# Kernel optimization log

Measured on AMD Instinct MI355X. Metric: run time of the kernel, lower is better.

Reference implementation:

```python
import jax, jax.numpy as jnp
import numpy as np

V, B, NP, NJ = 5, 32, 20, 17
NB = 16
ND = 128
POSE_MIN_DEPTH, POSE_MAX_DEPTH = 2000.0, 8000.0
POSE_SIGMA = 100.0
KS = 11
HIDDEN_ROUGH, HIDDEN = 1024, 1024
BONES = np.array([[0,1],[0,2],[1,3],[2,4],[5,6],[5,7],[7,9],[6,8],[8,10],[5,11],[6,12],[11,12],[11,13],[13,15],[12,14],[14,16]], dtype=np.int32)


def setup_inputs() -> dict:
    key = jax.random.key(0)
    ks = jax.random.split(key, 12)
    wh = jnp.array([1920.0, 1080.0], jnp.float32)
    kpts = jax.random.uniform(ks[0], (V, B, NP, NJ, 2), jnp.float32) * wh
    pose_vis = jnp.ones((V, B, NP), jnp.float32)
    joint_vis = (jax.random.uniform(ks[1], (V, B, NP, NJ)) > 0.15).astype(jnp.float32)
    gt_pose_depths = jax.random.uniform(ks[2], (B, NP), jnp.float32, 2000.0, 8000.0)
    gt_joint_depths = jax.random.uniform(ks[3], (B, NP, NJ), jnp.float32, -100.0, 100.0)
    angles = np.linspace(-0.3, 0.3, V)
    Rs = np.stack([np.array([[np.cos(a), 0.0, np.sin(a)], [0.0, 1.0, 0.0], [-np.sin(a), 0.0, np.cos(a)]], dtype=np.float32) for a in angles])
    cam_R = jnp.broadcast_to(jnp.asarray(Rs)[:, None], (V, B, 3, 3))
    tvec = np.zeros((V, 3), np.float32); tvec[:, 0] = np.linspace(-500.0, 500.0, V)
    cam_T = jnp.broadcast_to(jnp.asarray(tvec)[:, None], (V, B, 3))
    cam_f = jnp.full((V, B, 2), 1400.0, jnp.float32)
    cam_c = jnp.broadcast_to(jnp.array([960.0, 540.0], jnp.float32), (V, B, 2))
    image_wh = jnp.broadcast_to(jnp.array([1920.0, 1080.0], jnp.float32), (V, B, 2))
    num_persons = jax.random.randint(ks[4], (V, B), 10, NP + 1, jnp.int32)
    Wr1 = jax.random.normal(ks[5], (HIDDEN_ROUGH, NJ * 2)) * 0.02
    br1 = jnp.zeros((HIDDEN_ROUGH,), jnp.float32)
    Wr2 = jax.random.normal(ks[6], (NJ, HIDDEN_ROUGH)) * 0.02
    br2 = jnp.zeros((NJ,), jnp.float32)
    Wc1 = jax.random.normal(ks[7], (HIDDEN, NJ + NB, 3)) * 0.02
    bc1 = jnp.zeros((HIDDEN,), jnp.float32)
    Wc2 = jax.random.normal(ks[8], (1, HIDDEN, 3)) * 0.02
    bc2 = jnp.zeros((1,), jnp.float32)
    bones = jnp.asarray(BONES)
    return dict(kpts=kpts, pose_vis=pose_vis, joint_vis=joint_vis, gt_pose_depths=gt_pose_depths, gt_joint_depths=gt_joint_depths, cam_R=cam_R, cam_T=cam_T, cam_f=cam_f, cam_c=cam_c, image_wh=image_wh, num_persons=num_persons, Wr1=Wr1, br1=br1, Wr2=Wr2, br2=br2, Wc1=Wc1, bc1=bc1, Wc2=Wc2, bc2=bc2, bones=bones)


def _bone_len(p, bones):
    # p: [B, Np, Nj, D, 2] -> [B, Np, Nb, D]
    a = p[:, :, bones[:, 0]]
    b = p[:, :, bones[:, 1]]
    return jnp.sqrt(jnp.sum((a - b) ** 2, -1) + 1e-12)


def _conv1d(x, w, b):
    # x [N,C,L], w [O,I,3]
    y = jax.lax.conv_general_dilated(x, w, (1,), 'SAME', dimension_numbers=('NCH', 'OIH', 'NCH'))
    return y + b[None, :, None]


def _forward(kpts, joint_vis, cam_R, cam_T, cam_f, cam_c, image_wh, num_persons, Wr1, br1, Wr2, br2, Wc1, bc1, Wc2, bc2, bones):
    V_, B_, NP_, NJ_, _ = kpts.shape
    labels = jnp.arange(ND, dtype=jnp.float32) / (ND - 1) * (POSE_MAX_DEPTH - POSE_MIN_DEPTH) + POSE_MIN_DEPTH
    kt = kpts[0]  # target-view 2D poses [B,Np,Nj,2]
    # faithful to original indexing quirk: normalize all batches by batch-0 image size
    kn = kt / image_wh[0, 0][None, None, None, :]
    x = kn.reshape(B_ * NP_, NJ_ * 2)
    h = jax.nn.relu(x @ Wr1.T + br1)
    rough = (h @ Wr2.T + br2).reshape(B_, NP_, NJ_) * 1000.0
    rough = jax.lax.stop_gradient(rough)  # .detach() in original
    depths = labels[None, None, None, :] + rough[..., None]  # [B,Np,Nj,D]
    # back-project target 2D poses at every depth hypothesis
    R0, T0, f0, c0 = cam_R[0], cam_T[0], cam_f[0], cam_c[0]
    uvn = (kt - c0[:, None, None, :]) / f0[:, None, None, :]
    xy = uvn[..., None, :] * depths[..., None]
    cam_pts = jnp.concatenate([xy, depths[..., None]], -1)
    p3d = jnp.einsum('bji,bpkdj->bpkdi', R0, cam_pts) + T0[:, None, None, None, :]  # world [B,Np,Nj,D,3]

    scores = scores2 = boundings = boundings2 = None
    for rv in range(1, V_):
        Rr, Tr, fr, cr = cam_R[rv], cam_T[rv], cam_f[rv], cam_c[rv]
        xc = jnp.einsum('bij,bpkdj->bpkdi', Rr, p3d - Tr[:, None, None, None, :])
        p2t = xc[..., :2] / (xc[..., 2:3] + 1e-8) * fr[:, None, None, None, :] + cr[:, None, None, None, :]
        pr = kpts[rv]         # [B,Npr,Nj,2]
        vr = joint_vis[rv]    # [B,Npr,Nj]
        # pairwise dist over (target-person, ref-person) per joint/depth
        d = jnp.sum((p2t[:, :, None] - pr[:, None, :, :, None, :]) ** 2, -1)  # [B,Npt,Npr,Nj,D]
        w = vr[:, None, :, :, None]
        pdist = jnp.sum(d * w, 3) / (jnp.sum(w, 3) + 1e-8)  # [B,Npt,Npr,D]
        valid = jnp.arange(NP_)[None, None, :, None] < num_persons[rv][:, None, None, None]
        pdist = jnp.where(valid, pdist, 1e5)
        mm = jnp.argmin(pdist, 2)  # [B,Npt,D] nearest ref pose
        bidx = jnp.arange(B_)[:, None, None]
        matched = jnp.transpose(pr[bidx, mm], (0, 1, 3, 2, 4))  # [B,Npt,Nj,D,2]
        mvis = jnp.transpose(vr[bidx, mm], (0, 1, 3, 2))        # [B,Npt,Nj,D]
        mdist = jnp.sum((p2t - matched) ** 2, -1)
        score = jnp.exp(-jnp.sqrt(mdist + 1e-12) / POSE_SIGMA)  # panoptic branch
        score_bl = jnp.exp(-jnp.abs(_bone_len(matched, bones) - _bone_len(p2t, bones)) / 5.0)
        wimg = image_wh[rv][:, None, None, None, 0]
        himg = image_wh[rv][:, None, None, None, 1]
        inb = ((p2t[..., 0] >= 0) & (p2t[..., 1] >= 0) & (p2t[..., 0] <= wimg - 1) & (p2t[..., 1] <= himg - 1)).astype(score.dtype)
        bounding = inb * mvis
        bounding2 = jnp.broadcast_to(mvis[:, :, :1, :], score_bl.shape)
        if scores is None:
            scores, scores2 = score * bounding, score_bl * bounding2
            boundings, boundings2 = bounding, bounding2
        else:
            scores = scores + score * bounding
            scores2 = scores2 + score_bl * bounding2
            boundings = boundings + bounding
            boundings2 = boundings2 + bounding2
    psv = (scores / (boundings + 1e-8)).reshape(B_ * NP_, NJ_, ND)
    psv2 = (scores2 / (boundings2 + 1e-8)).reshape(B_ * NP_, NB, ND)
    xin = jnp.concatenate([psv, psv2], 1)  # [BN, Nj+Nb, D]
    hc = jax.nn.relu(_conv1d(xin, Wc1, bc1))
    logits = _conv1d(hc, Wc2, bc2)[:, 0, :]  # [BN, D]
    vol = jax.nn.softmax(logits, -1)
    # soft-argmax restricted to a window around the argmax
    pos = jnp.arange(ND, dtype=vol.dtype)
    idx = jnp.argmax(vol, -1)
    mask = (jnp.abs(pos[None, :] - idx[:, None].astype(vol.dtype)) <= KS // 2).astype(vol.dtype)
    mv = vol * mask
    mv = mv / (jnp.sum(mv, -1, keepdims=True) + 1e-8)
    pred_idx = jnp.sum(mv * pos, -1).reshape(B_, NP_)
    return pred_idx / (ND - 1) * (POSE_MAX_DEPTH - POSE_MIN_DEPTH) + POSE_MIN_DEPTH


def reference(kpts, pose_vis, joint_vis, gt_pose_depths, gt_joint_depths, cam_R, cam_T, cam_f, cam_c, image_wh, num_persons, Wr1, br1, Wr2, br2, Wc1, bc1, Wc2, bc2, bones):
    return _forward(kpts, joint_vis, cam_R, cam_T, cam_f, cam_c, image_wh, num_persons, Wr1, br1, Wr2, br2, Wc1, bc1, Wc2, bc2, bones)
```

## Files before the change

kernel.cpp:

```cpp
#include <hip/hip_runtime.h>
#include <math.h>

#define VV  5
#define BB  32
#define NPP 20
#define NJJ 17
#define NBB 16
#define NDD 128
#define HID 1024
#define KPITCH 128
#define PRP 36
#define VRP 20
#define NCH 34
#define RGH_P 20
#define BASE_P 52
#define A2_ELEMS (64 * 4 * 64 * 8)
#define EPI2_ELEMS (64 * 64 * 16)

typedef __attribute__((ext_vector_type(8))) short short8;
typedef __attribute__((ext_vector_type(4))) float floatx4;

static constexpr int BONE_A[NBB] = {0,0,1,2,5,5,7,6,8,5,6,11,11,13,12,14};
static constexpr int BONE_B[NBB] = {1,2,3,4,6,7,9,8,10,11,12,12,13,15,14,16};

__device__ __forceinline__ float warp_red_sum(float v) {
#pragma unroll
  for (int off = 32; off >= 1; off >>= 1) v += __shfl_xor(v, off, 64);
  return v;
}

__global__ __launch_bounds__(256) void prep_kernel(
    const float* __restrict__ Wc1, const float* __restrict__ Wc2,
    const float* __restrict__ bc1,
    unsigned short* __restrict__ A_hi, unsigned short* __restrict__ A_lo,
    float* __restrict__ epi) {
  int gidx = blockIdx.x * 256 + threadIdx.x;
  if (gidx < A2_ELEMS) {
    int e = gidx & 7;
    int l = (gidx >> 3) & 63;
    int rest = gidx >> 9;
    int ks = rest & 3;
    int ot = rest >> 2;
    int o = ot * 16 + (l & 15);
    int kk = ks * 32 + (l >> 4) * 8 + e;
    float x = (kk < 99) ? Wc1[o * 99 + kk] : 0.0f;
    unsigned int u = __float_as_uint(x);
    unsigned short hi = (unsigned short)(u >> 16);
    float xh = __uint_as_float((u >> 16) << 16);
    unsigned short lo = (unsigned short)(__float_as_uint(x - xh) >> 16);
    A_hi[gidx] = hi;
    A_lo[gidx] = lo;
  } else {
    int idx2 = gidx - A2_ELEMS;
    if (idx2 < EPI2_ELEMS) {
      int c = idx2 & 15;
      int l = (idx2 >> 4) & 63;
      int ot = idx2 >> 10;
      int base = ot * 16 + (l >> 4) * 4;
      epi[idx2] = (c < 12) ? Wc2[(base + c / 3) * 3 + (c % 3)] : bc1[base + (c - 12)];
    }
  }
}

__global__ __launch_bounds__(256) void pose_pre_kernel(
    const float* __restrict__ kpts, const float* __restrict__ cam_R,
    const float* __restrict__ cam_f, const float* __restrict__ cam_c,
    const float* __restrict__ image_wh,
    const float* __restrict__ Wr1, const float* __restrict__ br1,
    const float* __restrict__ Wr2, const float* __restrict__ br2,
    float* __restrict__ ws_rough, float* __restrict__ ws_base) {
  const int n = blockIdx.x;
  const int b = n / NPP;
  const int p = n % NPP;
  const int tid = threadIdx.x;
  const int wv = tid >> 6, ln = tid & 63;

  __shared__ float sh_x[NJJ * 2];
  __shared__ float sh_h[HID];

  if (tid < NJJ * 2) {
    int j = tid >> 1, c = tid & 1;
    float k = kpts[((size_t)(b * NPP + p)) * NJJ * 2 + j * 2 + c];
    sh_x[tid] = k / image_wh[c];
  }
  __syncthreads();

#pragma unroll
  for (int k = 0; k < 4; ++k) {
    int m = tid + k * 256;
    float acc = br1[m];
#pragma unroll
    for (int c = 0; c < NJJ * 2; ++c) acc = fmaf(Wr1[m * (NJJ * 2) + c], sh_x[c], acc);
    sh_h[m] = fmaxf(acc, 0.0f);
  }
  __syncthreads();

  for (int j = wv; j < NJJ; j += 4) {
    float part = 0.0f;
    for (int m = ln; m < HID; m += 64) part = fmaf(Wr2[j * HID + m], sh_h[m], part);
    part = warp_red_sum(part);
    if (ln == 0) ws_rough[(size_t)n * RGH_P + j] = (part + br2[j]) * 1000.0f;
  }

  if (tid < NJJ) {
    int j = tid;
    const float* R0 = cam_R + (size_t)b * 9;
    float c0x = cam_c[b * 2 + 0], c0y = cam_c[b * 2 + 1];
    float f0x = cam_f[b * 2 + 0], f0y = cam_f[b * 2 + 1];
    float kx = kpts[((size_t)(b * NPP + p)) * NJJ * 2 + j * 2 + 0];
    float ky = kpts[((size_t)(b * NPP + p)) * NJJ * 2 + j * 2 + 1];
    float ux = (kx - c0x) / f0x;
    float uy = (ky - c0y) / f0y;
#pragma unroll
    for (int i = 0; i < 3; ++i)
      ws_base[(size_t)n * BASE_P + j * 3 + i] =
          R0[0 * 3 + i] * ux + R0[1 * 3 + i] * uy + R0[2 * 3 + i];
  }
}

__global__ __launch_bounds__(256, 4) void pose_match_kernel(
    const float* __restrict__ kpts, const float* __restrict__ joint_vis,
    const float* __restrict__ cam_R, const float* __restrict__ cam_T,
    const float* __restrict__ cam_f, const float* __restrict__ cam_c,
    const float* __restrict__ image_wh, const int* __restrict__ num_persons,
    const float* __restrict__ ws_rough, const float* __restrict__ ws_base,
    float* __restrict__ ws_partial) {
  const int bid = blockIdx.x;
  const int n = bid >> 1;
  const int bh = bid & 1;
  const int b = n / NPP;
  const int tid = threadIdx.x;
  const int rvv = tid >> 6;
  const int d = bh * 64 + (tid & 63);

  __shared__ float sh_rough[NJJ];
  __shared__ float sh_base[NJJ][3];
  __shared__ __align__(16) float sh_pr[4][NPP][PRP];
  __shared__ __align__(16) float sh_vr[4][NPP][VRP];

  if (tid < NJJ) sh_rough[tid] = ws_rough[(size_t)n * RGH_P + tid];
  if (tid >= 64 && tid < 64 + NJJ * 3)
    ((float*)sh_base)[tid - 64] = ws_base[(size_t)n * BASE_P + (tid - 64)];

#pragma unroll
  for (int rr = 0; rr < 4; ++rr) {
    const float* prg = kpts + ((size_t)(rr + 1) * BB + b) * NPP * NJJ * 2;
    for (int idx = tid; idx < NPP * NJJ * 2; idx += 256)
      sh_pr[rr][idx / 34][idx % 34] = prg[idx];
    const float* vrg = joint_vis + ((size_t)(rr + 1) * BB + b) * NPP * NJJ;
    for (int idx = tid; idx < NPP * NJJ; idx += 256)
      sh_vr[rr][idx / 17][idx % 17] = vrg[idx];
  }
  if (tid < 4 * BB) {
    int rr = tid >> 5, q = tid & 31;
    if (q < NPP) {
      sh_pr[rr][q][34] = 0.0f; sh_pr[rr][q][35] = 0.0f;
      sh_vr[rr][q][17] = 0.0f; sh_vr[rr][q][18] = 0.0f; sh_vr[rr][q][19] = 0.0f;
    }
  }
  __syncthreads();

  {
    const int rv = rvv + 1;
    const int vb = rv * BB + b;
    const float* Rr = cam_R + (size_t)vb * 9;
    const float R00 = Rr[0], R01 = Rr[1], R02 = Rr[2];
    const float R10 = Rr[3], R11 = Rr[4], R12 = Rr[5];
    const float R20 = Rr[6], R21 = Rr[7], R22 = Rr[8];
    const float Trx = cam_T[vb * 3 + 0], Try = cam_T[vb * 3 + 1], Trz = cam_T[vb * 3 + 2];
    const float frx = cam_f[vb * 2 + 0], fry = cam_f[vb * 2 + 1];
    const float crx = cam_c[vb * 2 + 0], cry = cam_c[vb * 2 + 1];
    const float wmax = image_wh[vb * 2 + 0] - 1.0f;
    const float hmax = image_wh[vb * 2 + 1] - 1.0f;
    const int nprv = num_persons[vb];
    const float T0x = cam_T[b * 3 + 0], T0y = cam_T[b * 3 + 1], T0z = cam_T[b * 3 + 2];
    const float lab = ((float)d / 127.0f) * 6000.0f + 2000.0f;

    float px[NJJ], py[NJJ];
#pragma unroll
    for (int j = 0; j < NJJ; ++j) {
      float dep = lab + sh_rough[j];
      float p0 = fmaf(dep, sh_base[j][0], T0x);
      float p1 = fmaf(dep, sh_base[j][1], T0y);
      float p2 = fmaf(dep, sh_base[j][2], T0z);
      float q0 = p0 - Trx, q1 = p1 - Try, q2 = p2 - Trz;
      float xc0 = R00 * q0 + R01 * q1 + R02 * q2;
      float xc1 = R10 * q0 + R11 * q1 + R12 * q2;
      float xc2 = R20 * q0 + R21 * q1 + R22 * q2 + 1e-8f;
      px[j] = xc0 / xc2 * frx + crx;
      py[j] = xc1 / xc2 * fry + cry;
    }

    float best = 3.4e38f;
    int mm = 0;
#pragma unroll 1
    for (int q = 0; q < NPP; ++q) {
      const float4* pr4 = (const float4*)(&sh_pr[rvv][q][0]);
      const float4* vr4 = (const float4*)(&sh_vr[rvv][q][0]);
      float num = 0.0f, den = 0.0f;
#pragma unroll
      for (int g4 = 0; g4 < 4; ++g4) {
        float4 w  = vr4[g4];
        float4 pa = pr4[2 * g4 + 0];
        float4 pb = pr4[2 * g4 + 1];
        { float dx = px[4*g4+0] - pa.x, dy = py[4*g4+0] - pa.y; num = fmaf(w.x, dx*dx + dy*dy, num); den += w.x; }
        { float dx = px[4*g4+1] - pa.z, dy = py[4*g4+1] - pa.w; num = fmaf(w.y, dx*dx + dy*dy, num); den += w.y; }
        { float dx = px[4*g4+2] - pb.x, dy = py[4*g4+2] - pb.y; num = fmaf(w.z, dx*dx + dy*dy, num); den += w.z; }
        { float dx = px[4*g4+3] - pb.z, dy = py[4*g4+3] - pb.w; num = fmaf(w.w, dx*dx + dy*dy, num); den += w.w; }
      }
      {
        float w16 = sh_vr[rvv][q][16];
        float4 pc = pr4[8];
        float dx = px[16] - pc.x, dy = py[16] - pc.y;
        num = fmaf(w16, dx*dx + dy*dy, num); den += w16;
      }
      float pd = num / (den + 1e-8f);
      if (q >= nprv) pd = 100000.0f;
      if (pd < best) { best = pd; mm = q; }
    }

    float* pbase = ws_partial + (((size_t)n * NCH) * 4 + rvv) * 128 + d;
    unsigned int maskB = 0u;
#pragma unroll
    for (int j = 0; j < NJJ; ++j) {
      float mx = sh_pr[rvv][mm][j * 2 + 0];
      float my = sh_pr[rvv][mm][j * 2 + 1];
      float mv = sh_vr[rvv][mm][j];
      float dx = px[j] - mx, dy = py[j] - my;
      float sc = expf(-sqrtf(dx * dx + dy * dy + 1e-12f) / 100.0f);
      float inb = (px[j] >= 0.0f && py[j] >= 0.0f && px[j] <= wmax && py[j] <= hmax) ? 1.0f : 0.0f;
      float bd = inb * mv;
      pbase[j * 512] = sc * bd;
      maskB |= ((unsigned int)(bd != 0.0f)) << j;
    }
    float v0 = sh_vr[rvv][mm][0];
    maskB |= ((unsigned int)(v0 != 0.0f)) << 17;
#pragma unroll
    for (int nb = 0; nb < NBB; ++nb) {
      const int a = BONE_A[nb], c = BONE_B[nb];
      float ax = sh_pr[rvv][mm][a * 2 + 0], ay = sh_pr[rvv][mm][a * 2 + 1];
      float cx = sh_pr[rvv][mm][c * 2 + 0], cy = sh_pr[rvv][mm][c * 2 + 1];
      float dmx = ax - cx, dmy = ay - cy;
      float blm = sqrtf(dmx * dmx + dmy * dmy + 1e-12f);
      float dpx = px[a] - px[c], dpy = py[a] - py[c];
      float blp = sqrtf(dpx * dpx + dpy * dpy + 1e-12f);
      float scb = expf(-fabsf(blm - blp) / 5.0f);
      pbase[(NJJ + nb) * 512] = scb * v0;
    }
    *(unsigned int*)(pbase + 33 * 512) = maskB;
  }
}

__global__ __launch_bounds__(128) void reduce_kernel(
    const float* __restrict__ ws_partial, float* __restrict__ ws_xin) {
  const int n = blockIdx.x;
  const int t = threadIdx.x;
  const float* pb = ws_partial + ((size_t)n * NCH) * 4 * 128;
  float* xo = ws_xin + (size_t)n * (NJJ + NBB) * NDD;

  unsigned int m0 = __float_as_uint(pb[(33 * 4 + 0) * 128 + t]);
  unsigned int m1 = __float_as_uint(pb[(33 * 4 + 1) * 128 + t]);
  unsigned int m2 = __float_as_uint(pb[(33 * 4 + 2) * 128 + t]);
  unsigned int m3 = __float_as_uint(pb[(33 * 4 + 3) * 128 + t]);

#pragma unroll
  for (int i = 0; i < NJJ; ++i) {
    const float* a = pb + (i * 4) * 128 + t;
    float s = ((a[0] + a[128]) + a[256]) + a[384];
    int bj = ((m0 >> i) & 1) + ((m1 >> i) & 1) + ((m2 >> i) & 1) + ((m3 >> i) & 1);
    xo[i * NDD + t] = s / ((float)bj + 1e-8f);
  }
  int b2 = ((m0 >> 17) & 1) + ((m1 >> 17) & 1) + ((m2 >> 17) & 1) + ((m3 >> 17) & 1);
  float den2 = (float)b2 + 1e-8f;
#pragma unroll
  for (int nb = 0; nb < NBB; ++nb) {
    const float* a = pb + ((NJJ + nb) * 4) * 128 + t;
    float s = ((a[0] + a[128]) + a[256]) + a[384];
    xo[(NJJ + nb) * NDD + t] = s / den2;
  }
}

__global__ __launch_bounds__(512, 2) void conv_mfma_kernel(
    const float* __restrict__ ws_xin,
    const unsigned short* __restrict__ A_hi, const unsigned short* __restrict__ A_lo,
    const float* __restrict__ epi,
    const float* __restrict__ bc2, float* __restrict__ out) {
  const int n = blockIdx.x;
  const int tid = threadIdx.x;
  const int w = tid >> 6;
  const int l = tid & 63;
  const int lcol = l & 15;
  const int lg = l >> 4;

  __shared__ __align__(16) unsigned short bT_hi[128 * KPITCH];
  __shared__ __align__(16) unsigned short bT_lo[128 * KPITCH];
  __shared__ float plg[3][8][NDD];
  __shared__ float sh_l[NDD];
  __shared__ float sh_e[NDD];
  __shared__ float sh_sc[2];

  for (int i = tid; i < 3 * 8 * NDD; i += 512) ((float*)plg)[i] = 0.0f;

  const float* xn = ws_xin + (size_t)n * (NJJ + NBB) * NDD;
  for (int idx = tid; idx < 64 * 128; idx += 512) {
    const int kp = (idx & 63) << 1;
    const int t  = idx >> 6;
    unsigned int hp = 0, lp = 0;
#pragma unroll
    for (int u = 0; u < 2; ++u) {
      const int kk = kp + u;
      float x = 0.0f;
      if (kk < 99) {
        int i3 = kk / 3;
        int k3 = kk - i3 * 3;
        int tt = t + k3 - 1;
        if (tt >= 0 && tt < 128) x = xn[i3 * NDD + tt];
      }
      unsigned int uu = __float_as_uint(x);
      unsigned int hi = uu >> 16;
      float xh = __uint_as_float(hi << 16);
      unsigned int lo = __float_as_uint(x - xh) >> 16;
      hp |= hi << (16 * u);
      lp |= lo << (16 * u);
    }
    const int e = t * KPITCH + (kp ^ ((t & 15) << 3));
    *(unsigned int*)(bT_hi + e) = hp;
    *(unsigned int*)(bT_lo + e) = lp;
  }
  __syncthreads();

  const int sw = lcol << 3;

#pragma unroll 1
  for (int oi = 0; oi < 8; ++oi) {
    const int otg = w * 8 + oi;

    short8 Ah[4], Al[4];
    {
      const short8* ahT = ((const short8*)A_hi) + (size_t)otg * 4 * 64 + l;
      const short8* alT = ((const short8*)A_lo) + (size_t)otg * 4 * 64 + l;
#pragma unroll
      for (int ks = 0; ks < 4; ++ks) {
        Ah[ks] = ahT[ks * 64];
        Al[ks] = alT[ks * 64];
      }
    }
    float w2f[12];
    float bcf[4];
    {
      const float4* ep = ((const float4*)epi) + ((size_t)otg * 64 + l) * 4;
      float4 e0 = ep[0], e1 = ep[1], e2 = ep[2], e3 = ep[3];
      w2f[0] = e0.x; w2f[1] = e0.y; w2f[2] = e0.z; w2f[3] = e0.w;
      w2f[4] = e1.x; w2f[5] = e1.y; w2f[6] = e1.z; w2f[7] = e1.w;
      w2f[8] = e2.x; w2f[9] = e2.y; w2f[10] = e2.z; w2f[11] = e2.w;
      bcf[0] = e3.x; bcf[1] = e3.y; bcf[2] = e3.z; bcf[3] = e3.w;
    }

#pragma unroll 1
    for (int tp = 0; tp < 4; ++tp) {
      const int t0 = tp * 32 + lcol;
      const int t1 = t0 + 16;
      const unsigned short* b0h = bT_hi + t0 * KPITCH;
      const unsigned short* b1h = bT_hi + t1 * KPITCH;
      const unsigned short* b0l = bT_lo + t0 * KPITCH;
      const unsigned short* b1l = bT_lo + t1 * KPITCH;

      floatx4 X0 = {0.f, 0.f, 0.f, 0.f}, Y0 = {0.f, 0.f, 0.f, 0.f};
      floatx4 X1 = {0.f, 0.f, 0.f, 0.f}, Y1 = {0.f, 0.f, 0.f, 0.f};

#pragma unroll
      for (int ks = 0; ks < 4; ++ks) {
        const int e = (ks * 32 + lg * 8) ^ sw;
        short8 bh0 = *(const short8*)(b0h + e);
        short8 bh1 = *(const short8*)(b1h + e);
        X0 = __builtin_amdgcn_mfma_f32_16x16x32_bf16(Ah[ks], bh0, X0, 0, 0, 0);
        Y0 = __builtin_amdgcn_mfma_f32_16x16x32_bf16(Al[ks], bh0, Y0, 0, 0, 0);
        X1 = __builtin_amdgcn_mfma_f32_16x16x32_bf16(Ah[ks], bh1, X1, 0, 0, 0);
        Y1 = __builtin_amdgcn_mfma_f32_16x16x32_bf16(Al[ks], bh1, Y1, 0, 0, 0);
      }
#pragma unroll
      for (int ks = 0; ks < 4; ++ks) {
        const int e = (ks * 32 + lg * 8) ^ sw;
        short8 bl0 = *(const short8*)(b0l + e);
        short8 bl1 = *(const short8*)(b1l + e);
        if (ks & 1) {
          Y0 = __builtin_amdgcn_mfma_f32_16x16x32_bf16(Ah[ks], bl0, Y0, 0, 0, 0);
          Y1 = __builtin_amdgcn_mfma_f32_16x16x32_bf16(Ah[ks], bl1, Y1, 0, 0, 0);
        } else {
          X0 = __builtin_amdgcn_mfma_f32_16x16x32_bf16(Ah[ks], bl0, X0, 0, 0, 0);
          X1 = __builtin_amdgcn_mfma_f32_16x16x32_bf16(Ah[ks], bl1, X1, 0, 0, 0);
        }
      }

      {
        float sP = 0.0f, sC = 0.0f, sM = 0.0f;
#pragma unroll
        for (int r = 0; r < 4; ++r) {
          float h = fmaxf((X0[r] + Y0[r]) + bcf[r], 0.0f);
          sP = fmaf(h, w2f[r * 3 + 0], sP);
          sC = fmaf(h, w2f[r * 3 + 1], sC);
          sM = fmaf(h, w2f[r * 3 + 2], sM);
        }
        sP += __shfl_xor(sP, 16, 64); sP += __shfl_xor(sP, 32, 64);
        sC += __shfl_xor(sC, 16, 64); sC += __shfl_xor(sC, 32, 64);
        sM += __shfl_xor(sM, 16, 64); sM += __shfl_xor(sM, 32, 64);
        if (lg == 0) {
          plg[0][w][t0] += sP;
          plg[1][w][t0] += sC;
          plg[2][w][t0] += sM;
        }
      }
      {
        float sP = 0.0f, sC = 0.0f, sM = 0.0f;
#pragma unroll
        for (int r = 0; r < 4; ++r) {
          float h = fmaxf((X1[r] + Y1[r]) + bcf[r], 0.0f);
          sP = fmaf(h, w2f[r * 3 + 0], sP);
          sC = fmaf(h, w2f[r * 3 + 1], sC);
          sM = fmaf(h, w2f[r * 3 + 2], sM);
        }
        sP += __shfl_xor(sP, 16, 64); sP += __shfl_xor(sP, 32, 64);
        sC += __shfl_xor(sC, 16, 64); sC += __shfl_xor(sC, 32, 64);
        sM += __shfl_xor(sM, 16, 64); sM += __shfl_xor(sM, 32, 64);
        if (lg == 0) {
          plg[0][w][t1] += sP;
          plg[1][w][t1] += sC;
          plg[2][w][t1] += sM;
        }
      }
    }
  }
  __syncthreads();

  if (tid < NDD) {
    int t = tid;
    float lg2 = bc2[0];
#pragma unroll
    for (int ww = 0; ww < 8; ++ww) lg2 += plg[1][ww][t];
    if (t > 0) {
#pragma unroll
      for (int ww = 0; ww < 8; ++ww) lg2 += plg[0][ww][t - 1];
    }
    if (t < NDD - 1) {
#pragma unroll
      for (int ww = 0; ww < 8; ++ww) lg2 += plg[2][ww][t + 1];
    }
    sh_l[t] = lg2;
  }
  __syncthreads();
  if (tid < 64) {
    float v1 = sh_l[tid], v2 = sh_l[tid + 64];
    float mv; int mi;
    if (v2 > v1) { mv = v2; mi = tid + 64; } else { mv = v1; mi = tid; }
#pragma unroll
    for (int off = 32; off >= 1; off >>= 1) {
      float ov = __shfl_xor(mv, off, 64);
      int   oi2 = __shfl_xor(mi, off, 64);
      if (ov > mv || (ov == mv && oi2 < mi)) { mv = ov; mi = oi2; }
    }
    if (tid == 0) { sh_sc[0] = mv; ((int*)sh_sc)[1] = mi; }
  }
  __syncthreads();
  const float gmax = sh_sc[0];
  const int gidx = ((const int*)sh_sc)[1];
  if (tid < NDD) sh_e[tid] = expf(sh_l[tid] - gmax);
  __syncthreads();
  if (tid < 64) {
    float S = warp_red_sum(sh_e[tid] + sh_e[tid + 64]);
    float a1 = 0.0f, a2 = 0.0f;
#pragma unroll
    for (int k = 0; k < 2; ++k) {
      int t = tid + k * 64;
      float vol = sh_e[t] / S;
      float msk = (fabsf((float)t - (float)gidx) <= 5.0f) ? 1.0f : 0.0f;
      float mvv = vol * msk;
      a1 += mvv;
      a2 += mvv * (float)t;
    }
    a1 = warp_red_sum(a1);
    a2 = warp_red_sum(a2);
    if (tid == 0) {
      float pred = a2 / (a1 + 1e-8f);
      out[n] = pred / 127.0f * 6000.0f + 2000.0f;
    }
  }
}

extern "C" void kernel_launch(void* const* d_in, const int* in_sizes, int n_in,
                              void* d_out, int out_size, void* d_ws, size_t ws_size,
                              hipStream_t stream) {
  (void)in_sizes; (void)n_in; (void)out_size; (void)ws_size;
  const float* kpts        = (const float*)d_in[0];
  const float* joint_vis   = (const float*)d_in[2];
  const float* cam_R       = (const float*)d_in[5];
  const float* cam_T       = (const float*)d_in[6];
  const float* cam_f       = (const float*)d_in[7];
  const float* cam_c       = (const float*)d_in[8];
  const float* image_wh    = (const float*)d_in[9];
  const int*   num_persons = (const int*)d_in[10];
  const float* Wr1 = (const float*)d_in[11];
  const float* br1 = (const float*)d_in[12];
  const float* Wr2 = (const float*)d_in[13];
  const float* br2 = (const float*)d_in[14];
  const float* Wc1 = (const float*)d_in[15];
  const float* bc1 = (const float*)d_in[16];
  const float* Wc2 = (const float*)d_in[17];
  const float* bc2 = (const float*)d_in[18];
  float* out = (float*)d_out;

  unsigned short* A_hi = (unsigned short*)d_ws;
  unsigned short* A_lo = A_hi + A2_ELEMS;
  float* epi        = (float*)(A_lo + A2_ELEMS);
  float* ws_xin     = epi + EPI2_ELEMS;
  float* ws_partial = ws_xin + (size_t)BB * NPP * (NJJ + NBB) * NDD;
  float* ws_rough   = ws_partial + (size_t)BB * NPP * NCH * 4 * 128;
  float* ws_base    = ws_rough + (size_t)BB * NPP * RGH_P;

  const int prep_items = A2_ELEMS + EPI2_ELEMS;
  hipLaunchKernelGGL(prep_kernel, dim3((prep_items + 255) / 256), dim3(256), 0, stream,
                     Wc1, Wc2, bc1, A_hi, A_lo, epi);
  hipLaunchKernelGGL(pose_pre_kernel, dim3(BB * NPP), dim3(256), 0, stream,
                     kpts, cam_R, cam_f, cam_c, image_wh, Wr1, br1, Wr2, br2,
                     ws_rough, ws_base);
  hipLaunchKernelGGL(pose_match_kernel, dim3(BB * NPP * 2), dim3(256), 0, stream,
                     kpts, joint_vis, cam_R, cam_T, cam_f, cam_c, image_wh,
                     num_persons, ws_rough, ws_base, ws_partial);
  hipLaunchKernelGGL(reduce_kernel, dim3(BB * NPP), dim3(128), 0, stream,
                     ws_partial, ws_xin);
  hipLaunchKernelGGL(conv_mfma_kernel, dim3(BB * NPP), dim3(512), 0, stream,
                     ws_xin, A_hi, A_lo, epi, bc2, out);
}
```

Measured before the change: 193.9 us.

## Halve conv LDS staging by processing time axis in two halves, raise occupancy bounds

The conv MFMA kernel now stages the bf16 hi/lo split of the input in two 64-column halves instead of all 128 at once, halving the LDS footprint so more blocks can be resident per CU. Launch bounds are raised (conv 512 threads at 6 blocks, pose_match at 6) to push for higher occupancy. The cost is reloading the A-fragment weights and epilogue constants from global memory twice per block, plus extra barriers. The tighter register budget may also cause spills.

Result: slower. 289.4 us (+49.3%).

```diff
diff --git a/kernel.cpp b/kernel.cpp
--- a/kernel.cpp
+++ b/kernel.cpp
@@ -118,7 +118,7 @@
   }
 }
 
-__global__ __launch_bounds__(256, 4) void pose_match_kernel(
+__global__ __launch_bounds__(256, 6) void pose_match_kernel(
     const float* __restrict__ kpts, const float* __restrict__ joint_vis,
     const float* __restrict__ cam_R, const float* __restrict__ cam_T,
     const float* __restrict__ cam_f, const float* __restrict__ cam_c,
@@ -280,7 +280,7 @@
   }
 }
 
-__global__ __launch_bounds__(512, 2) void conv_mfma_kernel(
+__global__ __launch_bounds__(512, 6) void conv_mfma_kernel(
     const float* __restrict__ ws_xin,
     const unsigned short* __restrict__ A_hi, const unsigned short* __restrict__ A_lo,
     const float* __restrict__ epi,
@@ -292,8 +292,8 @@
   const int lcol = l & 15;
   const int lg = l >> 4;
 
-  __shared__ __align__(16) unsigned short bT_hi[128 * KPITCH];
-  __shared__ __align__(16) unsigned short bT_lo[128 * KPITCH];
+  __shared__ __align__(16) unsigned short bT_hi[64 * KPITCH];
+  __shared__ __align__(16) unsigned short bT_lo[64 * KPITCH];
   __shared__ float plg[3][8][NDD];
   __shared__ float sh_l[NDD];
   __shared__ float sh_e[NDD];
@@ -302,130 +302,136 @@
   for (int i = tid; i < 3 * 8 * NDD; i += 512) ((float*)plg)[i] = 0.0f;
 
   const float* xn = ws_xin + (size_t)n * (NJJ + NBB) * NDD;
-  for (int idx = tid; idx < 64 * 128; idx += 512) {
-    const int kp = (idx & 63) << 1;
-    const int t  = idx >> 6;
-    unsigned int hp = 0, lp = 0;
-#pragma unroll
-    for (int u = 0; u < 2; ++u) {
-      const int kk = kp + u;
-      float x = 0.0f;
-      if (kk < 99) {
-        int i3 = kk / 3;
-        int k3 = kk - i3 * 3;
-        int tt = t + k3 - 1;
-        if (tt >= 0 && tt < 128) x = xn[i3 * NDD + tt];
+  const int sw = lcol << 3;
+
+#pragma unroll 1
+  for (int half = 0; half < 2; ++half) {
+    __syncthreads();
+
+    for (int idx = tid; idx < 64 * 64; idx += 512) {
+      const int kp = (idx & 63) << 1;
+      const int tl = idx >> 6;
+      const int t = half * 64 + tl;
+      unsigned int hp = 0, lp = 0;
+#pragma unroll
+      for (int u = 0; u < 2; ++u) {
+        const int kk = kp + u;
+        float x = 0.0f;
+        if (kk < 99) {
+          int i3 = kk / 3;
+          int k3 = kk - i3 * 3;
+          int tt = t + k3 - 1;
+          if (tt >= 0 && tt < 128) x = xn[i3 * NDD + tt];
+        }
+        unsigned int uu = __float_as_uint(x);
+        unsigned int hi = uu >> 16;
+        float xh = __uint_as_float(hi << 16);
+        unsigned int lo = __float_as_uint(x - xh) >> 16;
+        hp |= hi << (16 * u);
+        lp |= lo << (16 * u);
       }
-      unsigned int uu = __float_as_uint(x);
-      unsigned int hi = uu >> 16;
-      float xh = __uint_as_float(hi << 16);
-      unsigned int lo = __float_as_uint(x - xh) >> 16;
-      hp |= hi << (16 * u);
-      lp |= lo << (16 * u);
-    }
-    const int e = t * KPITCH + (kp ^ ((t & 15) << 3));
-    *(unsigned int*)(bT_hi + e) = hp;
-    *(unsigned int*)(bT_lo + e) = lp;
-  }
-  __syncthreads();
-
-  const int sw = lcol << 3;
+      const int e = tl * KPITCH + (kp ^ ((tl & 15) << 3));
+      *(unsigned int*)(bT_hi + e) = hp;
+      *(unsigned int*)(bT_lo + e) = lp;
+    }
+    __syncthreads();
 
 #pragma unroll 1
-  for (int oi = 0; oi < 8; ++oi) {
-    const int otg = w * 8 + oi;
-
-    short8 Ah[4], Al[4];
-    {
-      const short8* ahT = ((const short8*)A_hi) + (size_t)otg * 4 * 64 + l;
-      const short8* alT = ((const short8*)A_lo) + (size_t)otg * 4 * 64 + l;
-#pragma unroll
-      for (int ks = 0; ks < 4; ++ks) {
-        Ah[ks] = ahT[ks * 64];
-        Al[ks] = alT[ks * 64];
-      }
-    }
-    float w2f[12];
-    float bcf[4];
-    {
-      const float4* ep = ((const float4*)epi) + ((size_t)otg * 64 + l) * 4;
-      float4 e0 = ep[0], e1 = ep[1], e2 = ep[2], e3 = ep[3];
-      w2f[0] = e0.x; w2f[1] = e0.y; w2f[2] = e0.z; w2f[3] = e0.w;
-      w2f[4] = e1.x; w2f[5] = e1.y; w2f[6] = e1.z; w2f[7] = e1.w;
-      w2f[8] = e2.x; w2f[9] = e2.y; w2f[10] = e2.z; w2f[11] = e2.w;
-      bcf[0] = e3.x; bcf[1] = e3.y; bcf[2] = e3.z; bcf[3] = e3.w;
-    }
-
-#pragma unroll 1
-    for (int tp = 0; tp < 4; ++tp) {
-      const int t0 = tp * 32 + lcol;
-      const int t1 = t0 + 16;
-      const unsigned short* b0h = bT_hi + t0 * KPITCH;
-      const unsigned short* b1h = bT_hi + t1 * KPITCH;
-      const unsigned short* b0l = bT_lo + t0 * KPITCH;
-      const unsigned short* b1l = bT_lo + t1 * KPITCH;
-
-      floatx4 X0 = {0.f, 0.f, 0.f, 0.f}, Y0 = {0.f, 0.f, 0.f, 0.f};
-      floatx4 X1 = {0.f, 0.f, 0.f, 0.f}, Y1 = {0.f, 0.f, 0.f, 0.f};
-
-#pragma unroll
-      for (int ks = 0; ks < 4; ++ks) {
-        const int e = (ks * 32 + lg * 8) ^ sw;
-        short8 bh0 = *(const short8*)(b0h + e);
-        short8 bh1 = *(const short8*)(b1h + e);
-        X0 = __builtin_amdgcn_mfma_f32_16x16x32_bf16(Ah[ks], bh0, X0, 0, 0, 0);
-        Y0 = __builtin_amdgcn_mfma_f32_16x16x32_bf16(Al[ks], bh0, Y0, 0, 0, 0);
-        X1 = __builtin_amdgcn_mfma_f32_16x16x32_bf16(Ah[ks], bh1, X1, 0, 0, 0);
-        Y1 = __builtin_amdgcn_mfma_f32_16x16x32_bf16(Al[ks], bh1, Y1, 0, 0, 0);
-      }
-#pragma unroll
-      for (int ks = 0; ks < 4; ++ks) {
-        const int e = (ks * 32 + lg * 8) ^ sw;
-        short8 bl0 = *(const short8*)(b0l + e);
-        short8 bl1 = *(const short8*)(b1l + e);
-        if (ks & 1) {
-          Y0 = __builtin_amdgcn_mfma_f32_16x16x32_bf16(Ah[ks], bl0, Y0, 0, 0, 0);
-          Y1 = __builtin_amdgcn_mfma_f32_16x16x32_bf16(Ah[ks], bl1, Y1, 0, 0, 0);
-        } else {
-          X0 = __builtin_amdgcn_mfma_f32_16x16x32_bf16(Ah[ks], bl0, X0, 0, 0, 0);
-          X1 = __builtin_amdgcn_mfma_f32_16x16x32_bf16(Ah[ks], bl1, X1, 0, 0, 0);
+    for (int oi = 0; oi < 8; ++oi) {
+      const int otg = w * 8 + oi;
+
+      short8 Ah[4], Al[4];
+      {
+        const short8* ahT = ((const short8*)A_hi) + (size_t)otg * 4 * 64 + l;
+        const short8* alT = ((const short8*)A_lo) + (size_t)otg * 4 * 64 + l;
+#pragma unroll
+        for (int ks = 0; ks < 4; ++ks) {
+          Ah[ks] = ahT[ks * 64];
+          Al[ks] = alT[ks * 64];
         }
       }
-
+      float w2f[12];
+      float bcf[4];
       {
-        float sP = 0.0f, sC = 0.0f, sM = 0.0f;
-#pragma unroll
-        for (int r = 0; r < 4; ++r) {
-          float h = fmaxf((X0[r] + Y0[r]) + bcf[r], 0.0f);
-          sP = fmaf(h, w2f[r * 3 + 0], sP);
-          sC = fmaf(h, w2f[r * 3 + 1], sC);
-          sM = fmaf(h, w2f[r * 3 + 2], sM);
+        const float4* ep = ((const float4*)epi) + ((size_t)otg * 64 + l) * 4;
+        float4 e0 = ep[0], e1 = ep[1], e2 = ep[2], e3 = ep[3];
+        w2f[0] = e0.x; w2f[1] = e0.y; w2f[2] = e0.z; w2f[3] = e0.w;
+        w2f[4] = e1.x; w2f[5] = e1.y; w2f[6] = e1.z; w2f[7] = e1.w;
+        w2f[8] = e2.x; w2f[9] = e2.y; w2f[10] = e2.z; w2f[11] = e2.w;
+        bcf[0] = e3.x; bcf[1] = e3.y; bcf[2] = e3.z; bcf[3] = e3.w;
+      }
+
+#pragma unroll 1
+      for (int tp = 0; tp < 2; ++tp) {
+        const int t0l = tp * 32 + lcol;
+        const int t1l = t0l + 16;
+        const unsigned short* b0h = bT_hi + t0l * KPITCH;
+        const unsigned short* b1h = bT_hi + t1l * KPITCH;
+        const unsigned short* b0l = bT_lo + t0l * KPITCH;
+        const unsigned short* b1l = bT_lo + t1l * KPITCH;
+
+        floatx4 X0 = {0.f, 0.f, 0.f, 0.f}, Y0 = {0.f, 0.f, 0.f, 0.f};
+        floatx4 X1 = {0.f, 0.f, 0.f, 0.f}, Y1 = {0.f, 0.f, 0.f, 0.f};
+
+#pragma unroll
+        for (int ks = 0; ks < 4; ++ks) {
+          const int e = (ks * 32 + lg * 8) ^ sw;
+          short8 bh0 = *(const short8*)(b0h + e);
+          short8 bh1 = *(const short8*)(b1h + e);
+          X0 = __builtin_amdgcn_mfma_f32_16x16x32_bf16(Ah[ks], bh0, X0, 0, 0, 0);
+          Y0 = __builtin_amdgcn_mfma_f32_16x16x32_bf16(Al[ks], bh0, Y0, 0, 0, 0);
+          X1 = __builtin_amdgcn_mfma_f32_16x16x32_bf16(Ah[ks], bh1, X1, 0, 0, 0);
+          Y1 = __builtin_amdgcn_mfma_f32_16x16x32_bf16(Al[ks], bh1, Y1, 0, 0, 0);
         }
-        sP += __shfl_xor(sP, 16, 64); sP += __shfl_xor(sP, 32, 64);
-        sC += __shfl_xor(sC, 16, 64); sC += __shfl_xor(sC, 32, 64);
-        sM += __shfl_xor(sM, 16, 64); sM += __shfl_xor(sM, 32, 64);
-        if (lg == 0) {
-          plg[0][w][t0] += sP;
-          plg[1][w][t0] += sC;
-          plg[2][w][t0] += sM;
+#pragma unroll
+        for (int ks = 0; ks < 4; ++ks) {
+          const int e = (ks * 32 + lg * 8) ^ sw;
+          short8 bl0 = *(const short8*)(b0l + e);
+          short8 bl1 = *(const short8*)(b1l + e);
+          if (ks & 1) {
+            Y0 = __builtin_amdgcn_mfma_f32_16x16x32_bf16(Ah[ks], bl0, Y0, 0, 0, 0);
+            Y1 = __builtin_amdgcn_mfma_f32_16x16x32_bf16(Ah[ks], bl1, Y1, 0, 0, 0);
+          } else {
+            X0 = __builtin_amdgcn_mfma_f32_16x16x32_bf16(Ah[ks], bl0, X0, 0, 0, 0);
+            X1 = __builtin_amdgcn_mfma_f32_16x16x32_bf16(Ah[ks], bl1, X1, 0, 0, 0);
+          }
         }
-      }
-      {
-        float sP = 0.0f, sC = 0.0f, sM = 0.0f;
-#pragma unroll
-        for (int r = 0; r < 4; ++r) {
-          float h = fmaxf((X1[r] + Y1[r]) + bcf[r], 0.0f);
-          sP = fmaf(h, w2f[r * 3 + 0], sP);
-          sC = fmaf(h, w2f[r * 3 + 1], sC);
-          sM = fmaf(h, w2f[r * 3 + 2], sM);
+
+        {
+          float sP = 0.0f, sC = 0.0f, sM = 0.0f;
+#pragma unroll
+          for (int r = 0; r < 4; ++r) {
+            float h = fmaxf((X0[r] + Y0[r]) + bcf[r], 0.0f);
+            sP = fmaf(h, w2f[r * 3 + 0], sP);
+            sC = fmaf(h, w2f[r * 3 + 1], sC);
+            sM = fmaf(h, w2f[r * 3 + 2], sM);
+          }
+          sP += __shfl_xor(sP, 16, 64); sP += __shfl_xor(sP, 32, 64);
+          sC += __shfl_xor(sC, 16, 64); sC += __shfl_xor(sC, 32, 64);
+          sM += __shfl_xor(sM, 16, 64); sM += __shfl_xor(sM, 32, 64);
+          if (lg == 0) {
+            plg[0][w][half * 64 + t0l] += sP;
+            plg[1][w][half * 64 + t0l] += sC;
+            plg[2][w][half * 64 + t0l] += sM;
+          }
         }
-        sP += __shfl_xor(sP, 16, 64); sP += __shfl_xor(sP, 32, 64);
-        sC += __shfl_xor(sC, 16, 64); sC += __shfl_xor(sC, 32, 64);
-        sM += __shfl_xor(sM, 16, 64); sM += __shfl_xor(sM, 32, 64);
-        if (lg == 0) {
-          plg[0][w][t1] += sP;
-          plg[1][w][t1] += sC;
-          plg[2][w][t1] += sM;
+        {
+          float sP = 0.0f, sC = 0.0f, sM = 0.0f;
+#pragma unroll
+          for (int r = 0; r < 4; ++r) {
+            float h = fmaxf((X1[r] + Y1[r]) + bcf[r], 0.0f);
+            sP = fmaf(h, w2f[r * 3 + 0], sP);
+            sC = fmaf(h, w2f[r * 3 + 1], sC);
+            sM = fmaf(h, w2f[r * 3 + 2], sM);
+          }
+          sP += __shfl_xor(sP, 16, 64); sP += __shfl_xor(sP, 32, 64);
+          sC += __shfl_xor(sC, 16, 64); sC += __shfl_xor(sC, 32, 64);
+          sM += __shfl_xor(sM, 16, 64); sM += __shfl_xor(sM, 32, 64);
+          if (lg == 0) {
+            plg[0][w][half * 64 + t1l] += sP;
+            plg[1][w][half * 64 + t1l] += sC;
+            plg[2][w][half * 64 + t1l] += sM;
+          }
         }
       }
     }
```
